# Optimization experiments

Hardware: AMD Instinct MI355X
Metric: run time of the kernel (lower is better)

Reference implementation:

```python
import jax, jax.numpy as jnp
import numpy as np
from jax import lax

# cell-group layout (order matters): sr_esoma, sr_edend, sr_pv, sr_sst, sr_vip, pfc_esoma, pfc_edend, pfc_pv, pfc_sst, pfc_vip
SIZES = [512, 1024, 128, 128, 128, 512, 1024, 128, 128, 128]
OFF = np.cumsum([0] + SIZES)
(SR_ES, SR_ED, SR_PV, SR_SST, SR_VIP,
 PFC_ES, PFC_ED, PFC_PV, PFC_SST, PFC_VIP) = [slice(int(OFF[i]), int(OFF[i + 1])) for i in range(10)]
N = int(OFF[-1])            # 3840 total neurons
N_BR = 2                    # dendritic branches per excitatory soma
N_IN, N_OUT = 128, 3
T, B = 100, 32
DT, TAU = 10.0, 50.0
DECAY = DT / TAU            # hp['dt']/hp['tau']
NOISE_STD = 0.01            # hp['network_noise']

# mGluR slow-integration coefficients on PFC E-dendrites: alpha_me = dt / logspace(100..5000), tiled over branches
_tau_me = np.tile(np.logspace(np.log10(100.0), np.log10(5000.0), SIZES[6] // N_BR), N_BR)
ALPHA_ME = jnp.asarray(DT / _tau_me, dtype=jnp.float32)   # [1024]

_dend = np.zeros(N, dtype=bool)
_dend[SR_ED] = True
_dend[PFC_ED] = True
DEND_VEC = jnp.asarray(_dend)


def _build_mask():
    """Dale's-law connectivity mask: +1 excitatory rows, -1 inhibitory rows,
    dend->own-region soma blocked (handled by dend2soma), zero diagonal."""
    m = np.ones((N, N), dtype=np.float32)
    for inh in (SR_PV, SR_SST, SR_VIP, PFC_PV, PFC_SST, PFC_VIP):
        m[inh, :] = -1.0
    m[SR_ED, SR_ES] = 0.0
    m[PFC_ED, PFC_ES] = 0.0
    np.fill_diagonal(m, 0.0)
    return m


def setup_inputs() -> dict:
    key = jax.random.key(0)
    ks = jax.random.split(key, 5)
    return {
        "x": jax.random.normal(ks[0], (T, B, N_IN), jnp.float32),
        "noise": jax.random.normal(ks[1], (T, B, N), jnp.float32),
        "w_rec": jax.random.normal(ks[2], (N, N), jnp.float32) / np.float32(np.sqrt(N)),
        "w_in": jax.random.normal(ks[3], (N_IN, N), jnp.float32) / np.float32(np.sqrt(N_IN)),
        "b": jnp.zeros((N,), jnp.float32),
        "d2s": jnp.ones((SIZES[1] + SIZES[6],), jnp.float32),
        "w_out": jax.random.normal(ks[4], (SIZES[0], N_OUT), jnp.float32) / np.float32(np.sqrt(SIZES[0])),
        "b_out": jnp.zeros((N_OUT,), jnp.float32),
        "mask": jnp.asarray(_build_mask()),
    }


def reference(x, noise, w_rec, w_in, b, d2s, w_out, b_out, mask):
    # effective recurrent weights: magnitude from w_rec, sign/sparsity from mask
    w_eff = jnp.abs(w_rec) * mask
    d2s_sr = d2s[:SIZES[1]].reshape(N_BR, SIZES[0])
    d2s_pfc = d2s[SIZES[1]:].reshape(N_BR, SIZES[5])
    nb = x.shape[1]
    h0 = jnp.zeros((nb, N), x.dtype)
    ime0 = jnp.zeros((nb, SIZES[6]), x.dtype)
    noise_scale = jnp.sqrt(jnp.asarray(2.0 * DECAY, x.dtype)) * NOISE_STD

    def step(carry, inp):
        h, ime = carry
        x_t, n_t = inp
        # rates: ReLU for somas/interneurons, sigmoidal dendritic nonlinearity for dendrites
        r = jnp.where(DEND_VEC[None, :], jax.nn.sigmoid(h), jax.nn.relu(h))
        pre = r @ w_eff + x_t @ w_in + b                      # [B, N]
        # dendrite -> soma coupling, summed over branches
        pre = pre.at[:, SR_ES].add(
            jnp.einsum('bkn,kn->bn', r[:, SR_ED].reshape(nb, N_BR, SIZES[0]), d2s_sr))
        pre = pre.at[:, PFC_ES].add(
            jnp.einsum('bkn,kn->bn', r[:, PFC_ED].reshape(nb, N_BR, SIZES[5]), d2s_pfc))
        # mGluR slow integration on PFC E-dendrites (per-dendrite time constants)
        ime_new = (1.0 - ALPHA_ME) * ime + ALPHA_ME * jax.nn.relu(pre[:, PFC_ED])
        pre = pre.at[:, PFC_ED].add(ime_new)
        # leaky integration with injected noise
        h_new = (1.0 - DECAY) * h + DECAY * pre + noise_scale * n_t
        out_t = r[:, SR_ES] @ w_out + b_out                   # readout from SR E somas
        return (h_new, ime_new), out_t

    _, outs = lax.scan(step, (h0, ime0), (x, noise))
    return outs   # [T, B, N_OUT]
```

## Files before the change

kernel.cpp:

```cpp
#include <hip/hip_runtime.h>
#include <math.h>

typedef _Float16 f16;
typedef f16 f16x8 __attribute__((ext_vector_type(8)));
typedef float f32x4 __attribute__((ext_vector_type(4)));

#define NTOT 3840
#define KP   3968
#define BATCH 32
#define TSTEPS 100
#define NIN 128
#define NWG 241
#define RSTRIDE (BATCH*KP)

__device__ __forceinline__ bool is_dend(int k){
  return (k>=512 && k<1536) || (k>=2432 && k<3456);
}
__device__ __forceinline__ bool is_inh(int k){
  return (k>=1536 && k<1920) || (k>=3456 && k<3840);
}
__device__ __forceinline__ ushort f2h(float v){ f16 h=(f16)v; return *(ushort*)&h; }
__device__ __forceinline__ float h2f(ushort u){ f16 h=*(f16*)&u; return (float)h; }

__global__ __launch_bounds__(256) void k_prep_w(const float* __restrict__ w_rec,
    const float* __restrict__ w_in, ushort* __restrict__ WT){
  __shared__ ushort tile[64][72];
  const int bid = blockIdx.x;
  const int kt = bid / 60, nt = bid % 60;
  const int k0 = kt*64, n0 = nt*64;
  const int t = threadIdx.x;
  const int tr = t>>2, tq = t&3;
  const int k = k0 + tr;
  const int cbase = n0 + tq*16;
  if (k < NTOT){
    const float sgn = is_inh(k) ? -1.f : 1.f;
    const bool rowSr  = (k>=512  && k<1536);
    const bool rowPfc = (k>=2432 && k<3456);
    #pragma unroll
    for (int q=0;q<4;q++){
      float4 w = *(const float4*)(w_rec + (size_t)k*NTOT + cbase + q*4);
      float v[4] = {sgn*fabsf(w.x), sgn*fabsf(w.y), sgn*fabsf(w.z), sgn*fabsf(w.w)};
      #pragma unroll
      for (int e=0;e<4;e++){
        const int n = cbase + q*4 + e;
        if (n==k || (rowSr && n<512) || (rowPfc && n>=1920 && n<2432)) v[e]=0.f;
        tile[tr][tq*16+q*4+e] = f2h(v[e]);
      }
    }
  } else {
    const float* src = w_in + (size_t)(k-NTOT)*NTOT + cbase;
    #pragma unroll
    for (int q=0;q<4;q++){
      float4 w = *(const float4*)(src + q*4);
      tile[tr][tq*16+q*4+0] = f2h(w.x);
      tile[tr][tq*16+q*4+1] = f2h(w.y);
      tile[tr][tq*16+q*4+2] = f2h(w.z);
      tile[tr][tq*16+q*4+3] = f2h(w.w);
    }
  }
  __syncthreads();
  const int n  = n0 + tr;
  const int kq = tq*16;
  uint u[8];
  #pragma unroll
  for (int q=0;q<8;q++)
    u[q] = (uint)tile[kq+2*q][tr] | ((uint)tile[kq+2*q+1][tr] << 16);
  uint4* dst = (uint4*)(WT + (size_t)n*KP + k0 + kq);
  dst[0] = make_uint4(u[0],u[1],u[2],u[3]);
  dst[1] = make_uint4(u[4],u[5],u[6],u[7]);
}

__global__ void k_init(const float* __restrict__ x, ushort* __restrict__ r0,
                       unsigned* __restrict__ bar){
  int i = blockIdx.x*blockDim.x + threadIdx.x;
  int nthr = gridDim.x*blockDim.x;
  for (int e=i; e<1024; e+=nthr) bar[e] = 0u;
  for (int e=i; e<BATCH*KP; e+=nthr){
    int b = e / KP, k = e % KP;
    float v = (k<NTOT) ? (is_dend(k)?0.5f:0.f) : x[b*NIN + (k-NTOT)];
    r0[e] = f2h(v);
  }
}

__global__ __launch_bounds__(512,1) void k_run(
    const ushort* __restrict__ WTu, ushort* rbase,
    const float* __restrict__ noise, const float* __restrict__ x,
    const float* __restrict__ bvec, const float* __restrict__ d2s,
    const float* __restrict__ w_out, const float* __restrict__ b_out,
    float* __restrict__ out, unsigned* bar)
{
  __shared__ ushort Blds[63488];
  __shared__ f32x4 red[3][2][64];
  const f16* WT = (const f16*)WTu;
  const int bid = blockIdx.x;
  const int tid = threadIdx.x;
  const int wv = tid>>6, l = tid&63, l15 = l&15, lh = l>>4;
  const int bh = wv&1, kw = wv>>1;
  const int n0 = bid*16;
  const int n  = n0 + l15;
  const int b0 = bh*16 + lh*4;
  const float NS = 0.0063245553203367585f;

  float hr[4] = {0.f,0.f,0.f,0.f};
  float im[4] = {0.f,0.f,0.f,0.f};
  float bv=0.f, dA=0.f, dB=0.f, al=0.f;
  bool cSR=false, cPFC=false, cME=false, dendF=false;
  if (bid < 240){
    if (kw == 0){
      bv = bvec[n];
      cSR  = (n0 < 512);
      cPFC = (n0 >= 1920 && n0 < 2432);
      cME  = (n0 >= 2432 && n0 < 3456);
      dendF = (n0>=512 && n0<1536) || cME;
      if (cSR){  dA=d2s[n];       dB=d2s[512+n]; }
      if (cPFC){ const int j=n-1920; dA=d2s[1024+j]; dB=d2s[1536+j]; }
      if (cME){
        const float LN10 = 2.302585092994046f;
        const float CEXP = 1.6989700043360187f/511.0f;
        const int j = n-2432;
        al = expf(-LN10*(1.0f + CEXP*(float)(j&511)));
      }
    }
    for (int c = tid; c < 16*496; c += 512){
      const int row = c / 496;
      const int kc  = c - row*496;
      f16x8 v = *(const f16x8*)(WT + (size_t)(n0+row)*KP + kc*8);
      *(f16x8*)((char*)Blds + kc*256 + row*16) = v;
    }
  }

  float wo[3][8];
  float bo0=0.f, bo1=0.f, bo2=0.f;
  if (bid == 240){
    #pragma unroll
    for (int o=0;o<3;o++)
      #pragma unroll
      for (int i=0;i<8;i++) wo[o][i] = w_out[(l*8+i)*3 + o];
    bo0 = b_out[0]; bo1 = b_out[1]; bo2 = b_out[2];
  }
  __syncthreads();

  const int xg = bid & 7;
  const unsigned mycnt = (xg==0) ? 31u : 30u;
  unsigned* xcnt = bar + xg*32;
  unsigned* xep  = bar + 256 + xg*32;
  unsigned* gcnt = bar + 512;

  const char* bb = (const char*)Blds + (kw*124 + lh)*256 + l15*16;

  for (int t=0; t<TSTEPS; t++){
    const ushort* rcu = rbase + (size_t)t*RSTRIDE;
    ushort*       rnu = rbase + (size_t)(t+1)*RSTRIDE;
    const f16* rc = (const f16*)rcu;

    if (bid < 240){
      float nz[4] = {0.f,0.f,0.f,0.f};
      float cA[4] = {0.f,0.f,0.f,0.f};
      float cB[4] = {0.f,0.f,0.f,0.f};
      if (kw == 0){
        #pragma unroll
        for (int rg=0;rg<4;rg++)
          nz[rg] = noise[(size_t)t*BATCH*NTOT + (b0+rg)*NTOT + n];
        if (cSR){
          #pragma unroll
          for (int rg=0;rg<4;rg++){
            cA[rg] = h2f(rcu[(b0+rg)*KP + 512 +n]);
            cB[rg] = h2f(rcu[(b0+rg)*KP + 1024+n]);
          }
        } else if (cPFC){
          const int j = n-1920;
          #pragma unroll
          for (int rg=0;rg<4;rg++){
            cA[rg] = h2f(rcu[(b0+rg)*KP + 2432+j]);
            cB[rg] = h2f(rcu[(b0+rg)*KP + 2944+j]);
          }
        }
      }

      f32x4 acc; acc.x=0.f; acc.y=0.f; acc.z=0.f; acc.w=0.f;
      {
        const f16* pa = rc + (size_t)(bh*16+l15)*KP + kw*992 + lh*8;
        #pragma unroll
        for (int ks=0; ks<31; ks++){
          f16x8 a = *(const f16x8*)(pa + ks*32);
          f16x8 b = *(const f16x8*)(bb + ks*1024);
          acc = __builtin_amdgcn_mfma_f32_16x16x32_f16(a, b, acc, 0,0,0);
        }
      }
      if (kw > 0) red[kw-1][bh][l] = acc;
      __syncthreads();
      if (kw == 0){
        #pragma unroll
        for (int w=0;w<3;w++) acc += red[w][bh][l];
        #pragma unroll
        for (int rg=0;rg<4;rg++){
          float p = acc[rg] + bv;
          p += cA[rg]*dA + cB[rg]*dB;
          if (cME){
            im[rg] = (1.f-al)*im[rg] + al*fmaxf(p,0.f); p += im[rg];
          }
          hr[rg] = 0.8f*hr[rg] + 0.2f*p + NS*nz[rg];
          const float rv = dendF ? (1.f/(1.f+expf(-hr[rg]))) : fmaxf(hr[rg],0.f);
          __hip_atomic_store(&rnu[(b0+rg)*KP + n], f2h(rv),
                             __ATOMIC_RELAXED, __HIP_MEMORY_SCOPE_AGENT);
        }
      }
    } else {
      #pragma unroll
      for (int q=0;q<12;q++){
        const int p = wv*12 + q;
        const int b = p/3, o = p%3;
        f16x8 rv8 = *(const f16x8*)(rc + (size_t)b*KP + l*8);
        float s = 0.f;
        #pragma unroll
        for (int i=0;i<8;i++) s += (float)rv8[i] * wo[o][i];
        #pragma unroll
        for (int off=32; off; off>>=1) s += __shfl_down(s, off);
        if (l==0){
          const float bo = (o==0)?bo0:((o==1)?bo1:bo2);
          out[t*BATCH*3 + b*3 + o] = s + bo;
        }
      }
      if (t+1 < TSTEPS && tid < 256){
        const int b = tid>>3, j = (tid&7)*16;
        const float* xs = x + (size_t)(t+1)*BATCH*NIN + b*NIN + j;
        #pragma unroll
        for (int q=0;q<4;q++){
          float4 v = *(const float4*)(xs + q*4);
          uint u0 = (uint)f2h(v.x) | ((uint)f2h(v.y)<<16);
          uint u1 = (uint)f2h(v.z) | ((uint)f2h(v.w)<<16);
          uint* dst = (uint*)&rnu[b*KP + NTOT + j + q*4];
          __hip_atomic_store(dst,   u0, __ATOMIC_RELAXED, __HIP_MEMORY_SCOPE_AGENT);
          __hip_atomic_store(dst+1, u1, __ATOMIC_RELAXED, __HIP_MEMORY_SCOPE_AGENT);
        }
      }
    }

    if (t+1 < TSTEPS){
      __syncthreads();
      if (tid == 0){
        unsigned old = __hip_atomic_fetch_add(xcnt, 1u,
                          __ATOMIC_RELAXED, __HIP_MEMORY_SCOPE_AGENT);
        if (old == mycnt*(unsigned)(t+1) - 1u){
          unsigned g = __hip_atomic_fetch_add(gcnt, 1u,
                          __ATOMIC_RELAXED, __HIP_MEMORY_SCOPE_AGENT);
          if (g == 8u*(unsigned)(t+1) - 1u){
            #pragma unroll
            for (int grp=0; grp<8; grp++)
              __hip_atomic_store(bar + 256 + grp*32, (unsigned)(t+1),
                            __ATOMIC_RELAXED, __HIP_MEMORY_SCOPE_AGENT);
          }
        }
        while (__hip_atomic_load(xep, __ATOMIC_RELAXED,
                      __HIP_MEMORY_SCOPE_AGENT) < (unsigned)(t+1))
          __builtin_amdgcn_s_sleep(1);
        asm volatile("" ::: "memory");
      }
      __syncthreads();
    }
  }
}

extern "C" void kernel_launch(void* const* d_in, const int* in_sizes, int n_in,
                              void* d_out, int out_size, void* d_ws, size_t ws_size,
                              hipStream_t stream) {
  const float* x     = (const float*)d_in[0];
  const float* noise = (const float*)d_in[1];
  const float* w_rec = (const float*)d_in[2];
  const float* w_in  = (const float*)d_in[3];
  const float* bvec  = (const float*)d_in[4];
  const float* d2s   = (const float*)d_in[5];
  const float* w_out = (const float*)d_in[6];
  const float* b_out = (const float*)d_in[7];
  float* out = (float*)d_out;

  char* ws = (char*)d_ws;
  ushort*   WT    = (ushort*)(ws);
  ushort*   rbase = (ushort*)(ws + 30474240);
  unsigned* bar   = (unsigned*)(ws + 56123392);

  k_prep_w<<<3720,256,0,stream>>>(w_rec, w_in, WT);
  k_init<<<64,256,0,stream>>>(x, rbase, bar);
  k_run<<<NWG,512,0,stream>>>(WT, rbase, noise, x, bvec, d2s,
                              w_out, b_out, out, bar);
}
```

Before: 964.7 us.

## Keep weight slices in registers and stage activation rows in LDS per step

Each workgroup now covers 32 output neurons for half the batch instead of 16 neurons for the full batch. Its weight slice stays in per-lane registers (31 f16x8 values) rather than LDS. Each timestep the workgroup cooperatively copies its 16 batch rows of the previous activations into LDS and feeds the MFMAs from there. Launch bounds now request 2 blocks per CU. The change removes the per-step global loads of activations by every wave, but adds a per-step LDS copy and an extra barrier, and raises register pressure.

```diff
diff --git a/kernel.cpp b/kernel.cpp
--- a/kernel.cpp
+++ b/kernel.cpp
@@ -82,22 +82,24 @@
   }
 }
 
-__global__ __launch_bounds__(512,1) void k_run(
+__global__ __launch_bounds__(512,2) void k_run(
     const ushort* __restrict__ WTu, ushort* rbase,
     const float* __restrict__ noise, const float* __restrict__ x,
     const float* __restrict__ bvec, const float* __restrict__ d2s,
     const float* __restrict__ w_out, const float* __restrict__ b_out,
     float* __restrict__ out, unsigned* bar)
 {
-  __shared__ ushort Blds[63488];
+  __shared__ ushort Alds[63488];
   __shared__ f32x4 red[3][2][64];
   const f16* WT = (const f16*)WTu;
   const int bid = blockIdx.x;
   const int tid = threadIdx.x;
   const int wv = tid>>6, l = tid&63, l15 = l&15, lh = l>>4;
-  const int bh = wv&1, kw = wv>>1;
-  const int n0 = bid*16;
-  const int n  = n0 + l15;
+  const int nh = wv&1, kw = wv>>1;
+  const int tile = bid>>1, bh = bid&1;
+  const int n0 = tile*32;
+  const int nsub = n0 + nh*16;
+  const int n  = nsub + l15;
   const int b0 = bh*16 + lh*4;
   const float NS = 0.0063245553203367585f;
 
@@ -105,13 +107,14 @@
   float im[4] = {0.f,0.f,0.f,0.f};
   float bv=0.f, dA=0.f, dB=0.f, al=0.f;
   bool cSR=false, cPFC=false, cME=false, dendF=false;
+  f16x8 breg[31];
   if (bid < 240){
     if (kw == 0){
       bv = bvec[n];
-      cSR  = (n0 < 512);
-      cPFC = (n0 >= 1920 && n0 < 2432);
-      cME  = (n0 >= 2432 && n0 < 3456);
-      dendF = (n0>=512 && n0<1536) || cME;
+      cSR  = (nsub < 512);
+      cPFC = (nsub >= 1920 && nsub < 2432);
+      cME  = (nsub >= 2432 && nsub < 3456);
+      dendF = (nsub>=512 && nsub<1536) || cME;
       if (cSR){  dA=d2s[n];       dB=d2s[512+n]; }
       if (cPFC){ const int j=n-1920; dA=d2s[1024+j]; dB=d2s[1536+j]; }
       if (cME){
@@ -121,12 +124,9 @@
         al = expf(-LN10*(1.0f + CEXP*(float)(j&511)));
       }
     }
-    for (int c = tid; c < 16*496; c += 512){
-      const int row = c / 496;
-      const int kc  = c - row*496;
-      f16x8 v = *(const f16x8*)(WT + (size_t)(n0+row)*KP + kc*8);
-      *(f16x8*)((char*)Blds + kc*256 + row*16) = v;
-    }
+    const f16* wb = WT + (size_t)(nsub + l15)*KP + kw*992 + lh*8;
+    #pragma unroll
+    for (int ks=0; ks<31; ks++) breg[ks] = *(const f16x8*)(wb + ks*32);
   }
 
   float wo[3][8];
@@ -138,7 +138,6 @@
       for (int i=0;i<8;i++) wo[o][i] = w_out[(l*8+i)*3 + o];
     bo0 = b_out[0]; bo1 = b_out[1]; bo2 = b_out[2];
   }
-  __syncthreads();
 
   const int xg = bid & 7;
   const unsigned mycnt = (xg==0) ? 31u : 30u;
@@ -146,7 +145,7 @@
   unsigned* xep  = bar + 256 + xg*32;
   unsigned* gcnt = bar + 512;
 
-  const char* bb = (const char*)Blds + (kw*124 + lh)*256 + l15*16;
+  const char* ab = (const char*)Alds + (kw*124 + lh)*256 + l15*16;
 
   for (int t=0; t<TSTEPS; t++){
     const ushort* rcu = rbase + (size_t)t*RSTRIDE;
@@ -154,6 +153,14 @@
     const f16* rc = (const f16*)rcu;
 
     if (bid < 240){
+      {
+        const f16* src = rc + (size_t)(bh*16)*KP;
+        for (int c = tid; c < 7936; c += 512){
+          const int row = c & 15, kc = c >> 4;
+          f16x8 v = *(const f16x8*)(src + (size_t)row*KP + kc*8);
+          *(f16x8*)((char*)Alds + kc*256 + row*16) = v;
+        }
+      }
       float nz[4] = {0.f,0.f,0.f,0.f};
       float cA[4] = {0.f,0.f,0.f,0.f};
       float cB[4] = {0.f,0.f,0.f,0.f};
@@ -176,22 +183,19 @@
           }
         }
       }
+      __syncthreads();
 
       f32x4 acc; acc.x=0.f; acc.y=0.f; acc.z=0.f; acc.w=0.f;
-      {
-        const f16* pa = rc + (size_t)(bh*16+l15)*KP + kw*992 + lh*8;
-        #pragma unroll
-        for (int ks=0; ks<31; ks++){
-          f16x8 a = *(const f16x8*)(pa + ks*32);
-          f16x8 b = *(const f16x8*)(bb + ks*1024);
-          acc = __builtin_amdgcn_mfma_f32_16x16x32_f16(a, b, acc, 0,0,0);
-        }
-      }
-      if (kw > 0) red[kw-1][bh][l] = acc;
+      #pragma unroll
+      for (int ks=0; ks<31; ks++){
+        f16x8 a = *(const f16x8*)(ab + ks*1024);
+        acc = __builtin_amdgcn_mfma_f32_16x16x32_f16(a, breg[ks], acc, 0,0,0);
+      }
+      if (kw > 0) red[kw-1][nh][l] = acc;
       __syncthreads();
       if (kw == 0){
         #pragma unroll
-        for (int w=0;w<3;w++) acc += red[w][bh][l];
+        for (int w=0;w<3;w++) acc += red[w][nh][l];
         #pragma unroll
         for (int rg=0;rg<4;rg++){
           float p = acc[rg] + bv;
```

After: 1.330 ms. 37.8% more time.
